# Optimization experiments

Hardware: AMD Instinct MI355X
Metric: run time of the kernel (lower is better)

The kernel has to match this reference:

```python
import jax, jax.numpy as jnp
import numpy as np

B, S, E, H, L = 4, 8192, 1024, 16, 64
D = E // H

def setup_inputs() -> dict:
    key = jax.random.key(0)
    ks = jax.random.split(key, 8)
    scale = 1.0 / np.sqrt(E)
    inp = {
        'query': jax.random.normal(ks[0], (B, S, E), jnp.float32),
        'key':   jax.random.normal(ks[1], (B, S, E), jnp.float32),
        'value': jax.random.normal(ks[2], (B, S, E), jnp.float32),
        'Wq': jax.random.normal(ks[3], (E, E), jnp.float32) * scale,
        'bq': jnp.zeros((E,), jnp.float32),
        'Wk': jax.random.normal(ks[4], (E, E), jnp.float32) * scale,
        'bk': jnp.zeros((E,), jnp.float32),
        'Wv': jax.random.normal(ks[5], (E, E), jnp.float32) * scale,
        'bv': jnp.zeros((E,), jnp.float32),
        'Wo': jax.random.normal(ks[6], (E, E), jnp.float32) * scale,
        'bo': jnp.zeros((E,), jnp.float32),
    }
    return inp

def reference(query, key, value, Wq, bq, Wk, bk, Wv, bv, Wo, bo):
    b, s, _ = query.shape
    # projections (torch Linear: x @ W.T + b), split heads -> [B, H, S, D]
    def split(x):
        return x.reshape(b, s, H, D).transpose(0, 2, 1, 3)
    q = split(query @ Wq.T + bq)
    k = split(key   @ Wk.T + bk)
    v = split(value @ Wv.T + bv)
    # landmark selection: key-norms averaged over heads -> [B, S], topk L per batch
    scores = jnp.linalg.norm(k, axis=-1).mean(axis=1)        # [B, S]
    _, idx = jax.lax.top_k(scores, L)                        # [B, L]
    # gather landmark K/V -> [B, H, L, D]
    gidx = idx[:, None, :, None]                             # [B, 1, L, 1]
    k_sp = jnp.take_along_axis(k, gidx, axis=2)
    v_sp = jnp.take_along_axis(v, gidx, axis=2)
    # attention over landmarks only
    attn = jnp.einsum('bhsd,bhld->bhsl', q, k_sp) / jnp.sqrt(jnp.asarray(D, q.dtype))
    w = jax.nn.softmax(attn, axis=-1)                        # [B, H, S, L]
    out = jnp.einsum('bhsl,bhld->bhsd', w, v_sp)             # [B, H, S, D]
    out = out.transpose(0, 2, 1, 3).reshape(b, s, E)
    out = out @ Wo.T + bo
    return (out, w)
```

## Files before the change

kernel.cpp:

```cpp
#include <hip/hip_runtime.h>
#include <cstdint>

typedef unsigned short u16;
typedef __attribute__((ext_vector_type(8))) short short8;
typedef __attribute__((ext_vector_type(4))) float f32x4;

#define AS1 __attribute__((address_space(1)))
#define AS3 __attribute__((address_space(3)))

#define BB 4
#define SS 8192
#define EE 1024
#define HH 16
#define DD 64
#define LL 64
#define CANDN 96

__device__ __forceinline__ void async16(const void* g, void* l) {
  __builtin_amdgcn_global_load_lds((const AS1 uint32_t*)g, (AS3 uint32_t*)l, 16, 0, 0);
}
__device__ __forceinline__ u16 f2b(float f) {
  uint32_t u = __float_as_uint(f);
  return (u16)((u + 0x7fffu + ((u >> 16) & 1u)) >> 16);
}
__device__ __forceinline__ float b2f(u16 h) { return __uint_as_float(((uint32_t)h) << 16); }

__global__ __launch_bounds__(256) void cvt_bf16_k(const float* __restrict__ in, u16* __restrict__ out, int n4) {
  int i = blockIdx.x * 256 + threadIdx.x;
  if (i >= n4) return;
  float4 v = ((const float4*)in)[i];
  ushort4 o;
  o.x = f2b(v.x); o.y = f2b(v.y); o.z = f2b(v.z); o.w = f2b(v.w);
  ((ushort4*)out)[i] = o;
}

#define FENCE_RW()  asm volatile("s_waitcnt lgkmcnt(0)\n\ts_barrier" ::: "memory")
#define FENCE_V6()  asm volatile("s_waitcnt vmcnt(6)\n\ts_barrier" ::: "memory")
#define FENCE_V0()  asm volatile("s_waitcnt vmcnt(0)\n\ts_barrier" ::: "memory")

__global__ __launch_bounds__(512) void gemm256(const u16* __restrict__ A, const u16* __restrict__ W,
                                               const float* __restrict__ bias,
                                               float* __restrict__ Cf, u16* __restrict__ Cb,
                                               float* __restrict__ scA, int K) {
  extern __shared__ __align__(16) u16 lds_[];
  u16* lA = lds_;
  u16* lB = lds_ + 32768;
  const int tid = threadIdx.x;
  const int wv = tid >> 6, lane = tid & 63;
  const int quad = lane >> 4, l15 = lane & 15;
  const int wm = wv >> 1, wn = wv & 1;

  const int nwg = gridDim.x * gridDim.y;
  int g = blockIdx.y * gridDim.x + blockIdx.x;
  int bx = blockIdx.x, by = blockIdx.y;
  if ((nwg & 7) == 0) {
    const int chunk = nwg >> 3;
    const int v = (g & 7) * chunk + (g >> 3);
    bx = v % gridDim.x;
    by = v / gridDim.x;
  }
  const int mt = by * 256, nt = bx * 128;

  const int rl = tid >> 3;
  const int g8 = (((tid & 7) ^ (rl & 7))) * 8;
  const u16* sA00 = A + (size_t)(mt + rl) * K + g8;
  const u16* sA01 = A + (size_t)(mt + 64 + rl) * K + g8;
  const u16* sA10 = A + (size_t)(mt + 128 + rl) * K + g8;
  const u16* sA11 = A + (size_t)(mt + 192 + rl) * K + g8;
  const u16* sB0  = W + (size_t)(nt + rl) * K + g8;
  const u16* sB1  = W + (size_t)(nt + 64 + rl) * K + g8;
  const int dA = tid * 8;
  const int dB = tid * 8;

  auto STAGE = [&](int tile, int pb) {
    const int off = tile * 64;
    async16(sA00 + off, lA + pb * 16384 + dA);
    async16(sA01 + off, lA + pb * 16384 + dA + 4096);
    async16(sA10 + off, lA + pb * 16384 + 8192 + dA);
    async16(sA11 + off, lA + pb * 16384 + 8192 + dA + 4096);
    async16(sB0 + off, lB + pb * 8192 + dB);
    async16(sB1 + off, lB + pb * 8192 + dB + 4096);
  };

  f32x4 acc[4][4];
#pragma unroll
  for (int i = 0; i < 4; i++)
#pragma unroll
    for (int j = 0; j < 4; j++) acc[i][j] = (f32x4){0.f, 0.f, 0.f, 0.f};

  const int NT = K >> 6;
  STAGE(0, 0);
  STAGE(1, 1);
  FENCE_V6();

  for (int t = 0; t < NT; ++t) {
    const int pb = t & 1;
    const short8* pA = (const short8*)(lA + pb * 16384);
    const short8* pB = (const short8*)(lB + pb * 8192);
    short8 af[2][4], bf[2][4];
#pragma unroll
    for (int i = 0; i < 4; i++) {
      const int r = 64 * wm + 16 * i + l15;
      af[0][i] = pA[r * 8 + (quad ^ (r & 7))];
      af[1][i] = pA[r * 8 + ((quad + 4) ^ (r & 7))];
      const int rb = 64 * wn + 16 * i + l15;
      bf[0][i] = pB[rb * 8 + (quad ^ (rb & 7))];
      bf[1][i] = pB[rb * 8 + ((quad + 4) ^ (rb & 7))];
    }
#pragma unroll
    for (int i = 0; i < 4; i++)
#pragma unroll
      for (int j = 0; j < 4; j++)
        acc[i][j] = __builtin_amdgcn_mfma_f32_16x16x32_bf16(af[0][i], bf[0][j], acc[i][j], 0, 0, 0);
    FENCE_RW();
    if (t + 2 < NT) STAGE(t + 2, pb);
#pragma unroll
    for (int i = 0; i < 4; i++)
#pragma unroll
      for (int j = 0; j < 4; j++)
        acc[i][j] = __builtin_amdgcn_mfma_f32_16x16x32_bf16(af[1][i], bf[1][j], acc[i][j], 0, 0, 0);
    if (t + 1 < NT) {
      if (t + 1 == NT - 1) { FENCE_V0(); } else { FENCE_V6(); }
    }
  }

  float bs[4];
#pragma unroll
  for (int j = 0; j < 4; j++) bs[j] = bias[nt + 64 * wn + 16 * j + l15];
#pragma unroll
  for (int i = 0; i < 4; i++) {
#pragma unroll
    for (int r = 0; r < 4; r++) {
      const int gm = mt + 64 * wm + 16 * i + quad * 4 + r;
      float nrm = 0.f;
#pragma unroll
      for (int j = 0; j < 4; j++) {
        float v = acc[i][j][r] + bs[j];
        const int gn = nt + 64 * wn + 16 * j + l15;
        if (Cf) Cf[(size_t)gm * EE + gn] = v;
        if (Cb) Cb[(size_t)gm * EE + gn] = f2b(v);
        nrm += v * v;
      }
      if (scA) {
#pragma unroll
        for (int m = 1; m < 16; m <<= 1) nrm += __shfl_xor(nrm, m, 64);
        if (l15 == 0) atomicAdd(&scA[gm], sqrtf(nrm) * (1.f / 16.f));
      }
    }
  }
}

#define TKT 1024
#define EQCAP 256
__global__ __launch_bounds__(TKT) void topk1_k(const float* __restrict__ sc, int* __restrict__ cand) {
  const int b = blockIdx.x;
  __shared__ uint32_t s[SS];
  __shared__ int wsum[TKT / 64];
  __shared__ int cnt_sh;
  __shared__ int counter, eqcount;
  __shared__ int eqbuf[EQCAP];
  const int tid = threadIdx.x;
  const int lane = tid & 63, wv = tid >> 6;
  for (int i = tid; i < SS; i += TKT) s[i] = __float_as_uint(sc[b * SS + i]);
  if (tid == 0) { counter = 0; eqcount = 0; }
  __syncthreads();

  uint32_t lo = 0u, hi = 0x7f7fffffu;
  while (lo < hi) {
    uint32_t mid = lo + ((hi - lo + 1) >> 1);
    int c = 0;
    for (int i = tid; i < SS; i += TKT) c += (s[i] >= mid) ? 1 : 0;
#pragma unroll
    for (int m = 1; m < 64; m <<= 1) c += __shfl_xor(c, m, 64);
    if (lane == 0) wsum[wv] = c;
    __syncthreads();
    if (tid == 0) {
      int t = 0;
#pragma unroll
      for (int w = 0; w < TKT / 64; w++) t += wsum[w];
      cnt_sh = t;
    }
    __syncthreads();
    if (cnt_sh >= CANDN) lo = mid; else hi = mid - 1;
    __syncthreads();
  }
  const uint32_t T = lo;

  for (int i = tid; i < SS; i += TKT) {
    uint32_t u = s[i];
    if (u > T) {
      int p = atomicAdd(&counter, 1);
      cand[b * CANDN + p] = i;
    } else if (u == T) {
      int p = atomicAdd(&eqcount, 1);
      if (p < EQCAP) eqbuf[p] = i;
    }
  }
  __syncthreads();
  const int above = counter;
  const int rem = CANDN - above;
  int ec = eqcount; if (ec > EQCAP) ec = EQCAP;
  __syncthreads();
  for (int i = tid; i < ec; i += TKT) {
    int me = eqbuf[i];
    int rank = 0;
    for (int j = 0; j < ec; j++) rank += (eqbuf[j] < me) ? 1 : 0;
    if (rank < rem) {
      int p = atomicAdd(&counter, 1);
      cand[b * CANDN + p] = me;
    }
  }
}

__global__ __launch_bounds__(256) void rescore_k(const float* __restrict__ key, const float* __restrict__ Wk,
                                                 const int* __restrict__ cand, double* __restrict__ kpart) {
  const int kc = blockIdx.x, h = blockIdx.y, b = blockIdx.z;
  const int d = threadIdx.x & 63, cg = threadIdx.x >> 6;
  __shared__ float wk[64 * 257];
  __shared__ float xs[24 * 256];
  for (int i = threadIdx.x; i < 64 * 256; i += 256)
    wk[(i >> 8) * 257 + (i & 255)] = Wk[(size_t)(h * 64 + (i >> 8)) * EE + kc * 256 + (i & 255)];
  for (int c0 = 0; c0 < CANDN; c0 += 24) {
    __syncthreads();
    for (int i = threadIdx.x; i < 24 * 256; i += 256) {
      int c = c0 + (i >> 8);
      xs[i] = key[((size_t)b * SS + cand[b * CANDN + c]) * EE + kc * 256 + (i & 255)];
    }
    __syncthreads();
    double acc[6] = {0, 0, 0, 0, 0, 0};
    for (int kk = 0; kk < 256; kk++) {
      double wv_ = (double)wk[d * 257 + kk];
#pragma unroll
      for (int j = 0; j < 6; j++)
        acc[j] += wv_ * (double)xs[(cg * 6 + j) * 256 + kk];
    }
#pragma unroll
    for (int j = 0; j < 6; j++) {
      int c = c0 + cg * 6 + j;
      kpart[(((size_t)kc * BB + b) * CANDN + c) * 1024 + h * 64 + d] = acc[j];
    }
  }
}

__global__ __launch_bounds__(64) void score2_k(const double* __restrict__ kpart, const float* __restrict__ bk,
                                               double* __restrict__ sc2) {
  const int c = blockIdx.x, b = blockIdx.y;
  const int lane = threadIdx.x;
  double tot = 0.0;
  for (int h = 0; h < HH; h++) {
    double v = (double)bk[h * 64 + lane];
#pragma unroll
    for (int kc = 0; kc < 4; kc++)
      v += kpart[(((size_t)kc * BB + b) * CANDN + c) * 1024 + h * 64 + lane];
    double s = v * v;
#pragma unroll
    for (int m = 1; m < 64; m <<= 1) s += __shfl_xor(s, m, 64);
    tot += sqrt(s);
  }
  if (lane == 0) sc2[b * CANDN + c] = tot * (1.0 / 16.0);
}

__global__ __launch_bounds__(128) void topk2_k(const double* __restrict__ sc2, const int* __restrict__ cand,
                                               int* __restrict__ idxf) {
  const int b = blockIdx.x, t = threadIdx.x;
  if (t >= CANDN) return;
  double my = sc2[b * CANDN + t];
  int mi = cand[b * CANDN + t];
  int rank = 0;
  for (int j = 0; j < CANDN; j++) {
    double sj = sc2[b * CANDN + j];
    int ij = cand[b * CANDN + j];
    if (sj > my || (sj == my && ij < mi)) rank++;
  }
  if (rank < LL) idxf[b * LL + rank] = mi;
}

__global__ __launch_bounds__(256) void gatherx_k(const float* __restrict__ value, const int* __restrict__ idxf,
                                                 u16* __restrict__ xg) {
  const int r = blockIdx.x;
  const int b = r >> 6;
  const float* src = value + ((size_t)b * SS + idxf[r]) * EE;
  for (int i = threadIdx.x; i < EE; i += 256) xg[(size_t)r * EE + i] = f2b(src[i]);
}

__global__ __launch_bounds__(64) void gathersp_k(const u16* __restrict__ kb, const float* __restrict__ vg,
                                                 const int* __restrict__ idxf,
                                                 u16* __restrict__ ksp, u16* __restrict__ vspT) {
  const int g = blockIdx.x;
  const int l = g & 63, h = (g >> 6) & 15, b = g >> 10;
  const int d = threadIdx.x;
  ksp[(size_t)g * 64 + d] = kb[((size_t)b * SS + idxf[b * 64 + l]) * EE + h * 64 + d];
  vspT[((size_t)(b * 16 + h) * 64 + d) * 64 + l] = f2b(vg[((size_t)b * 64 + l) * EE + h * 64 + d]);
}

__global__ __launch_bounds__(256) void attn_k(const u16* __restrict__ qb, const u16* __restrict__ ksp,
                                              const u16* __restrict__ vspT,
                                              float* __restrict__ wout, u16* __restrict__ attnb) {
  __shared__ __align__(16) u16 qt[4096];
  __shared__ __align__(16) u16 kt[4096];
  __shared__ __align__(16) u16 vt[4096];
  __shared__ __align__(16) u16 wt[4096];
  const int tid = threadIdx.x;
  const int wv = tid >> 6, lane = tid & 63, quad = lane >> 4, l15 = lane & 15;
  const int s0 = blockIdx.x * 64;
  const int bh = blockIdx.y, b = bh >> 4, h = bh & 15;

  {
    const int bi0 = tid, bi1 = 256 + tid;
    const int r0 = bi0 >> 3, c0 = (bi0 & 7) ^ (r0 & 7);
    const int r1 = bi1 >> 3, c1 = (bi1 & 7) ^ (r1 & 7);
    const u16* qg = qb + ((size_t)b * SS + s0) * EE + h * 64;
    async16(qg + (size_t)r0 * EE + c0 * 8, qt + bi0 * 8);
    async16(qg + (size_t)r1 * EE + c1 * 8, qt + bi1 * 8);
    const u16* kg = ksp + (size_t)bh * 4096;
    async16(kg + r0 * 64 + c0 * 8, kt + bi0 * 8);
    async16(kg + r1 * 64 + c1 * 8, kt + bi1 * 8);
    const u16* vgp = vspT + (size_t)bh * 4096;
    async16(vgp + r0 * 64 + c0 * 8, vt + bi0 * 8);
    async16(vgp + r1 * 64 + c1 * 8, vt + bi1 * 8);
  }
  __syncthreads();

  f32x4 acc[4];
#pragma unroll
  for (int j = 0; j < 4; j++) acc[j] = (f32x4){0.f, 0.f, 0.f, 0.f};
  const int ar = 16 * wv + l15;
#pragma unroll
  for (int ks = 0; ks < 2; ks++) {
    const int cg = quad + ks * 4;
    short8 af = ((const short8*)qt)[ar * 8 + (cg ^ (ar & 7))];
#pragma unroll
    for (int j = 0; j < 4; j++) {
      int br = 16 * j + l15;
      short8 bf = ((const short8*)kt)[br * 8 + (cg ^ (br & 7))];
      acc[j] = __builtin_amdgcn_mfma_f32_16x16x32_bf16(af, bf, acc[j], 0, 0, 0);
    }
  }
#pragma unroll
  for (int j = 0; j < 4; j++) acc[j] *= 0.125f;

  float inv[4];
#pragma unroll
  for (int r = 0; r < 4; r++) {
    float m = fmaxf(fmaxf(acc[0][r], acc[1][r]), fmaxf(acc[2][r], acc[3][r]));
#pragma unroll
    for (int msk = 1; msk < 16; msk <<= 1) m = fmaxf(m, __shfl_xor(m, msk, 64));
    float e0 = __expf(acc[0][r] - m);
    float e1 = __expf(acc[1][r] - m);
    float e2 = __expf(acc[2][r] - m);
    float e3 = __expf(acc[3][r] - m);
    acc[0][r] = e0; acc[1][r] = e1; acc[2][r] = e2; acc[3][r] = e3;
    float s = e0 + e1 + e2 + e3;
#pragma unroll
    for (int msk = 1; msk < 16; msk <<= 1) s += __shfl_xor(s, msk, 64);
    inv[r] = 1.f / s;
  }

  const size_t wbase = ((size_t)bh * SS + s0 + 16 * wv) * 64;
#pragma unroll
  for (int j = 0; j < 4; j++) {
#pragma unroll
    for (int r = 0; r < 4; r++) {
      float val = acc[j][r] * inv[r];
      int rowl = quad * 4 + r;
      int l = 16 * j + l15;
      wout[wbase + (size_t)rowl * 64 + l] = val;
      int wr = 16 * wv + rowl;
      wt[wr * 64 + ((l >> 3) ^ (wr & 7)) * 8 + (l & 7)] = f2b(val);
    }
  }
  __syncthreads();

  f32x4 acc2[4];
#pragma unroll
  for (int j = 0; j < 4; j++) acc2[j] = (f32x4){0.f, 0.f, 0.f, 0.f};
#pragma unroll
  for (int ks = 0; ks < 2; ks++) {
    const int cg = quad + ks * 4;
    short8 af = ((const short8*)wt)[ar * 8 + (cg ^ (ar & 7))];
#pragma unroll
    for (int j = 0; j < 4; j++) {
      int br = 16 * j + l15;
      short8 bf = ((const short8*)vt)[br * 8 + (cg ^ (br & 7))];
      acc2[j] = __builtin_amdgcn_mfma_f32_16x16x32_bf16(af, bf, acc2[j], 0, 0, 0);
    }
  }
#pragma unroll
  for (int j = 0; j < 4; j++)
#pragma unroll
    for (int r = 0; r < 4; r++)
      attnb[((size_t)b * SS + s0 + 16 * wv + quad * 4 + r) * EE + h * 64 + 16 * j + l15] = f2b(acc2[j][r]);
}

extern "C" void kernel_launch(void* const* d_in, const int* in_sizes, int n_in,
                              void* d_out, int out_size, void* d_ws, size_t ws_size,
                              hipStream_t stream) {
  (void)in_sizes; (void)n_in; (void)out_size; (void)ws_size;
  const float* query = (const float*)d_in[0];
  const float* key   = (const float*)d_in[1];
  const float* value = (const float*)d_in[2];
  const float* Wq = (const float*)d_in[3];
  const float* bq = (const float*)d_in[4];
  const float* Wk = (const float*)d_in[5];
  const float* bk = (const float*)d_in[6];
  const float* Wv = (const float*)d_in[7];
  const float* bv = (const float*)d_in[8];
  const float* Wo = (const float*)d_in[9];
  const float* bo = (const float*)d_in[10];
  float* out = (float*)d_out;
  float* wout = out + (size_t)BB * SS * EE;

  char* p = (char*)d_ws;
  auto alloc = [&](size_t n) { char* r = p; p += (n + 255) & ~(size_t)255; return r; };
  u16* qbf = (u16*)alloc((size_t)BB * SS * EE * 2);
  u16* kbf = (u16*)alloc((size_t)BB * SS * EE * 2);
  u16* wqb = (u16*)alloc((size_t)EE * EE * 2);
  u16* wkb = (u16*)alloc((size_t)EE * EE * 2);
  u16* wvb = (u16*)alloc((size_t)EE * EE * 2);
  u16* wob = (u16*)alloc((size_t)EE * EE * 2);
  u16* qb  = (u16*)alloc((size_t)BB * SS * EE * 2);
  u16* kb  = (u16*)alloc((size_t)BB * SS * EE * 2);
  float*  sc    = (float*)alloc((size_t)BB * SS * 4);
  int*    cand  = (int*)alloc(BB * CANDN * 4);
  double* kpart = (double*)alloc((size_t)4 * BB * CANDN * 1024 * 8);
  double* sc2   = (double*)alloc(BB * CANDN * 8);
  int*    idxf  = (int*)alloc(BB * LL * 4);
  u16*    xg    = (u16*)alloc((size_t)BB * LL * EE * 2);
  float*  vg    = (float*)alloc((size_t)BB * LL * EE * 4);
  u16*    ksp   = (u16*)alloc((size_t)BB * HH * LL * DD * 2);
  u16*    vspT  = (u16*)alloc((size_t)BB * HH * DD * LL * 2);
  u16*    attnb = qbf;

  const int M = BB * SS;
  const size_t gemm_lds = 98304;

  cvt_bf16_k<<<(M * EE / 4 + 255) / 256, 256, 0, stream>>>(query, qbf, M * EE / 4);
  cvt_bf16_k<<<(M * EE / 4 + 255) / 256, 256, 0, stream>>>(key, kbf, M * EE / 4);
  cvt_bf16_k<<<(EE * EE / 4 + 255) / 256, 256, 0, stream>>>(Wq, wqb, EE * EE / 4);
  cvt_bf16_k<<<(EE * EE / 4 + 255) / 256, 256, 0, stream>>>(Wk, wkb, EE * EE / 4);
  cvt_bf16_k<<<(EE * EE / 4 + 255) / 256, 256, 0, stream>>>(Wv, wvb, EE * EE / 4);
  cvt_bf16_k<<<(EE * EE / 4 + 255) / 256, 256, 0, stream>>>(Wo, wob, EE * EE / 4);
  hipMemsetAsync(sc, 0, (size_t)M * 4, stream);

  dim3 gg(EE / 128, M / 256);
  gemm256<<<gg, 512, gemm_lds, stream>>>(qbf, wqb, bq, nullptr, qb, nullptr, EE);
  gemm256<<<gg, 512, gemm_lds, stream>>>(kbf, wkb, bk, nullptr, kb, sc, EE);

  topk1_k<<<BB, TKT, 0, stream>>>(sc, cand);
  rescore_k<<<dim3(4, HH, BB), 256, 0, stream>>>(key, Wk, cand, kpart);
  score2_k<<<dim3(CANDN, BB), 64, 0, stream>>>(kpart, bk, sc2);
  topk2_k<<<BB, 128, 0, stream>>>(sc2, cand, idxf);

  gatherx_k<<<BB * LL, 256, 0, stream>>>(value, idxf, xg);
  gemm256<<<dim3(EE / 128, BB * LL / 256), 512, gemm_lds, stream>>>(xg, wvb, bv, vg, nullptr, nullptr, EE);
  gathersp_k<<<BB * HH * LL, 64, 0, stream>>>(kb, vg, idxf, ksp, vspT);

  attn_k<<<dim3(SS / 64, BB * HH), 256, 0, stream>>>(qb, ksp, vspT, wout, attnb);

  gemm256<<<gg, 512, gemm_lds, stream>>>(attnb, wob, bo, out, nullptr, nullptr, EE);
}
```

Measured before the change: 979.8 us.

## Replace GEMM with 256x256 tile kernel using interleaved load/MFMA ping-pong schedule

Replaces the 256x128 double-buffered GEMM with a 256x256 tile kernel. Each of 8 waves computes 128x64 outputs, and the K-loop is split into four MFMA quadrants interleaved with LDS reads and partial async global->LDS stages. Barriers use sched_barrier and s_setprio around the MFMA blocks. The goal is better compute/load overlap and more reuse per tile, at the cost of 128KB LDS (one block per CU), more accumulator registers, and fewer workgroups.

```diff
diff --git a/kernel.cpp b/kernel.cpp
--- a/kernel.cpp
+++ b/kernel.cpp
@@ -34,21 +34,17 @@
   ((ushort4*)out)[i] = o;
 }
 
-#define FENCE_RW()  asm volatile("s_waitcnt lgkmcnt(0)\n\ts_barrier" ::: "memory")
-#define FENCE_V6()  asm volatile("s_waitcnt vmcnt(6)\n\ts_barrier" ::: "memory")
-#define FENCE_V0()  asm volatile("s_waitcnt vmcnt(0)\n\ts_barrier" ::: "memory")
-
-__global__ __launch_bounds__(512) void gemm256(const u16* __restrict__ A, const u16* __restrict__ W,
-                                               const float* __restrict__ bias,
-                                               float* __restrict__ Cf, u16* __restrict__ Cb,
-                                               float* __restrict__ scA, int K) {
+#define SBAR() { __builtin_amdgcn_sched_barrier(0); __builtin_amdgcn_s_barrier(); __builtin_amdgcn_sched_barrier(0); }
+
+__global__ __launch_bounds__(512) void gemm8p(const u16* __restrict__ A, const u16* __restrict__ W,
+                                              const float* __restrict__ bias,
+                                              float* __restrict__ Cf, u16* __restrict__ Cb,
+                                              float* __restrict__ scA, int K) {
   extern __shared__ __align__(16) u16 lds_[];
-  u16* lA = lds_;
-  u16* lB = lds_ + 32768;
   const int tid = threadIdx.x;
   const int wv = tid >> 6, lane = tid & 63;
   const int quad = lane >> 4, l15 = lane & 15;
-  const int wm = wv >> 1, wn = wv & 1;
+  const int wm = wv >> 2, wn = wv & 3;
 
   const int nwg = gridDim.x * gridDim.y;
   int g = blockIdx.y * gridDim.x + blockIdx.x;
@@ -59,84 +55,93 @@
     bx = v % gridDim.x;
     by = v / gridDim.x;
   }
-  const int mt = by * 256, nt = bx * 128;
+  const int mt = by * 256, nt = bx * 256;
 
   const int rl = tid >> 3;
   const int g8 = (((tid & 7) ^ (rl & 7))) * 8;
-  const u16* sA00 = A + (size_t)(mt + rl) * K + g8;
-  const u16* sA01 = A + (size_t)(mt + 64 + rl) * K + g8;
-  const u16* sA10 = A + (size_t)(mt + 128 + rl) * K + g8;
-  const u16* sA11 = A + (size_t)(mt + 192 + rl) * K + g8;
-  const u16* sB0  = W + (size_t)(nt + rl) * K + g8;
-  const u16* sB1  = W + (size_t)(nt + 64 + rl) * K + g8;
-  const int dA = tid * 8;
-  const int dB = tid * 8;
-
-  auto STAGE = [&](int tile, int pb) {
-    const int off = tile * 64;
-    async16(sA00 + off, lA + pb * 16384 + dA);
-    async16(sA01 + off, lA + pb * 16384 + dA + 4096);
-    async16(sA10 + off, lA + pb * 16384 + 8192 + dA);
-    async16(sA11 + off, lA + pb * 16384 + 8192 + dA + 4096);
-    async16(sB0 + off, lB + pb * 8192 + dB);
-    async16(sB1 + off, lB + pb * 8192 + dB + 4096);
-  };
-
-  f32x4 acc[4][4];
-#pragma unroll
-  for (int i = 0; i < 4; i++)
+  const u16* sA[4]; const u16* sB[4];
+#pragma unroll
+  for (int c = 0; c < 4; c++) {
+    sA[c] = A + (size_t)(mt + c * 64 + rl) * K + g8;
+    sB[c] = W + (size_t)(nt + c * 64 + rl) * K + g8;
+  }
+  const short8* L8 = (const short8*)lds_;
+
+  f32x4 acc[8][4];
+#pragma unroll
+  for (int i = 0; i < 8; i++)
 #pragma unroll
     for (int j = 0; j < 4; j++) acc[i][j] = (f32x4){0.f, 0.f, 0.f, 0.f};
 
   const int NT = K >> 6;
-  STAGE(0, 0);
-  STAGE(1, 1);
-  FENCE_V6();
-
-  for (int t = 0; t < NT; ++t) {
-    const int pb = t & 1;
-    const short8* pA = (const short8*)(lA + pb * 16384);
-    const short8* pB = (const short8*)(lB + pb * 8192);
-    short8 af[2][4], bf[2][4];
-#pragma unroll
-    for (int i = 0; i < 4; i++) {
-      const int r = 64 * wm + 16 * i + l15;
-      af[0][i] = pA[r * 8 + (quad ^ (r & 7))];
-      af[1][i] = pA[r * 8 + ((quad + 4) ^ (r & 7))];
-      const int rb = 64 * wn + 16 * i + l15;
-      bf[0][i] = pB[rb * 8 + (quad ^ (rb & 7))];
-      bf[1][i] = pB[rb * 8 + ((quad + 4) ^ (rb & 7))];
-    }
-#pragma unroll
-    for (int i = 0; i < 4; i++)
-#pragma unroll
-      for (int j = 0; j < 4; j++)
-        acc[i][j] = __builtin_amdgcn_mfma_f32_16x16x32_bf16(af[0][i], bf[0][j], acc[i][j], 0, 0, 0);
-    FENCE_RW();
-    if (t + 2 < NT) STAGE(t + 2, pb);
-#pragma unroll
-    for (int i = 0; i < 4; i++)
-#pragma unroll
-      for (int j = 0; j < 4; j++)
-        acc[i][j] = __builtin_amdgcn_mfma_f32_16x16x32_bf16(af[1][i], bf[1][j], acc[i][j], 0, 0, 0);
-    if (t + 1 < NT) {
-      if (t + 1 == NT - 1) { FENCE_V0(); } else { FENCE_V6(); }
-    }
+  const int gp0 = (0 * 4 + quad) ^ (l15 & 7);
+  const int gp1 = (1 * 4 + quad) ^ (l15 & 7);
+
+#define STA(T, D, C) async16(sA[C] + (T) * 64, lds_ + (D) * 16384 + (C) * 4096 + tid * 8)
+#define STB(T, D, C) async16(sB[C] + (T) * 64, lds_ + 32768 + (D) * 16384 + (C) * 4096 + tid * 8)
+#define RDA(D, RH) { _Pragma("unroll") for (int i = 0; i < 4; i++) { \
+    const int bidx = (D) * 2048 + (2 * wm + (RH)) * 512 + (16 * i + l15) * 8; \
+    af[0][i] = L8[bidx + gp0]; af[1][i] = L8[bidx + gp1]; } }
+#define RDB(D, CH, BF) { _Pragma("unroll") for (int j = 0; j < 2; j++) { \
+    const int bidx = 4096 + (D) * 2048 + wn * 512 + ((CH) * 32 + 16 * j + l15) * 8; \
+    BF[0][j] = L8[bidx + gp0]; BF[1][j] = L8[bidx + gp1]; } }
+#define MFMA_Q(RH, CH, BF) { __builtin_amdgcn_s_setprio(1); \
+    _Pragma("unroll") for (int i = 0; i < 4; i++) \
+      _Pragma("unroll") for (int j = 0; j < 2; j++) { \
+        acc[(RH)*4+i][(CH)*2+j] = __builtin_amdgcn_mfma_f32_16x16x32_bf16(af[0][i], BF[0][j], acc[(RH)*4+i][(CH)*2+j], 0, 0, 0); \
+        acc[(RH)*4+i][(CH)*2+j] = __builtin_amdgcn_mfma_f32_16x16x32_bf16(af[1][i], BF[1][j], acc[(RH)*4+i][(CH)*2+j], 0, 0, 0); } \
+    __builtin_amdgcn_s_setprio(0); }
+
+  STA(0, 0, 0); STA(0, 0, 2);
+  STB(0, 0, 0); STB(0, 0, 1);
+  STB(0, 0, 2); STB(0, 0, 3);
+  STA(0, 0, 1); STA(0, 0, 3);
+  if (NT > 1) {
+    STA(1, 1, 0); STA(1, 1, 2);
+    STB(1, 1, 0); STB(1, 1, 1);
+    STB(1, 1, 2); STB(1, 1, 3);
+  }
+  asm volatile("s_waitcnt vmcnt(8)" ::: "memory");
+  SBAR();
+
+  for (int kt = 0; kt < NT; ++kt) {
+    const int d = kt & 1, o = d ^ 1;
+    short8 af[2][4], bf0[2][2], bf1[2][2];
+    RDA(d, 0);
+    RDB(d, 0, bf0);
+    if (kt + 1 < NT) { STA(kt + 1, o, 1); STA(kt + 1, o, 3); }
+    SBAR();
+    MFMA_Q(0, 0, bf0);
+    RDB(d, 1, bf1);
+    if (kt + 2 < NT) { STA(kt + 2, d, 0); STA(kt + 2, d, 2); }
+    if (kt < NT - 2)       { asm volatile("s_waitcnt vmcnt(10)" ::: "memory"); }
+    else if (kt == NT - 2) { asm volatile("s_waitcnt vmcnt(8)" ::: "memory"); }
+    else                   { asm volatile("s_waitcnt vmcnt(0)" ::: "memory"); }
+    SBAR();
+    MFMA_Q(0, 1, bf1);
+    RDA(d, 1);
+    if (kt + 2 < NT) { STB(kt + 2, d, 0); STB(kt + 2, d, 1); }
+    SBAR();
+    MFMA_Q(1, 1, bf1);
+    if (kt + 2 < NT) { STB(kt + 2, d, 2); STB(kt + 2, d, 3); }
+    if (kt + 2 < NT)      { asm volatile("s_waitcnt vmcnt(8)" ::: "memory"); SBAR(); }
+    else if (kt + 1 < NT) { asm volatile("s_waitcnt vmcnt(2)" ::: "memory"); SBAR(); }
+    MFMA_Q(1, 0, bf0);
   }
 
   float bs[4];
 #pragma unroll
-  for (int j = 0; j < 4; j++) bs[j] = bias[nt + 64 * wn + 16 * j + l15];
-#pragma unroll
-  for (int i = 0; i < 4; i++) {
+  for (int j = 0; j < 4; j++) bs[j] = bias[nt + wn * 64 + 16 * j + l15];
+#pragma unroll
+  for (int i = 0; i < 8; i++) {
 #pragma unroll
     for (int r = 0; r < 4; r++) {
-      const int gm = mt + 64 * wm + 16 * i + quad * 4 + r;
+      const int gm = mt + wm * 128 + 16 * i + quad * 4 + r;
       float nrm = 0.f;
 #pragma unroll
       for (int j = 0; j < 4; j++) {
         float v = acc[i][j][r] + bs[j];
-        const int gn = nt + 64 * wn + 16 * j + l15;
+        const int gn = nt + wn * 64 + 16 * j + l15;
         if (Cf) Cf[(size_t)gm * EE + gn] = v;
         if (Cb) Cb[(size_t)gm * EE + gn] = f2b(v);
         nrm += v * v;
@@ -432,7 +437,7 @@
   u16*    attnb = qbf;
 
   const int M = BB * SS;
-  const size_t gemm_lds = 98304;
+  const size_t g8p_lds = 131072;
 
   cvt_bf16_k<<<(M * EE / 4 + 255) / 256, 256, 0, stream>>>(query, qbf, M * EE / 4);
   cvt_bf16_k<<<(M * EE / 4 + 255) / 256, 256, 0, stream>>>(key, kbf, M * EE / 4);
@@ -442,9 +447,9 @@
   cvt_bf16_k<<<(EE * EE / 4 + 255) / 256, 256, 0, stream>>>(Wo, wob, EE * EE / 4);
   hipMemsetAsync(sc, 0, (size_t)M * 4, stream);
 
-  dim3 gg(EE / 128, M / 256);
-  gemm256<<<gg, 512, gemm_lds, stream>>>(qbf, wqb, bq, nullptr, qb, nullptr, EE);
-  gemm256<<<gg, 512, gemm_lds, stream>>>(kbf, wkb, bk, nullptr, kb, sc, EE);
+  dim3 gg(EE / 256, M / 256);
+  gemm8p<<<gg, 512, g8p_lds, stream>>>(qbf, wqb, bq, nullptr, qb, nullptr, EE);
+  gemm8p<<<gg, 512, g8p_lds, stream>>>(kbf, wkb, bk, nullptr, kb, sc, EE);
 
   topk1_k<<<BB, TKT, 0, stream>>>(sc, cand);
   rescore_k<<<dim3(4, HH, BB), 256, 0, stream>>>(key, Wk, cand, kpart);
@@ -452,10 +457,10 @@
   topk2_k<<<BB, 128, 0, stream>>>(sc2, cand, idxf);
 
   gatherx_k<<<BB * LL, 256, 0, stream>>>(value, idxf, xg);
-  gemm256<<<dim3(EE / 128, BB * LL / 256), 512, gemm_lds, stream>>>(xg, wvb, bv, vg, nullptr, nullptr, EE);
+  gemm8p<<<dim3(EE / 256, BB * LL / 256), 512, g8p_lds, stream>>>(xg, wvb, bv, vg, nullptr, nullptr, EE);
   gathersp_k<<<BB * HH * LL, 64, 0, stream>>>(kb, vg, idxf, ksp, vspT);
 
   attn_k<<<dim3(SS / 64, BB * HH), 256, 0, stream>>>(qb, ksp, vspT, wout, attnb);
 
-  gemm256<<<gg, 512, gemm_lds, stream>>>(attnb, wob, bo, out, nullptr, nullptr, EE);
-}
+  gemm8p<<<gg, 512, g8p_lds, stream>>>(attnb, wob, bo, out, nullptr, nullptr, EE);
+}
```

Result: faster. 920.8 us (-6.0%).
